# Performance work log

Measured on AMD Instinct MI355X. Metric: run time of the kernel, lower is better.

## Reference

```python
import jax, jax.numpy as jnp
import numpy as np

N_ATOMS = 30000
N_PAIRS = 1200000
N_BASIS = 7
N_RADIAL = 5
N_SPECIES = 119
R_MIN = 0.5
R_MAX = 6.0
UNITS = (512, 512)
BOX = 6.0  # Angstrom box edge so many pairs fall inside the cutoff
N_FEAT = 360  # gaussian-moment feature count for n_radial=5

# static triangular index sets (fully symmetric contractions)
_TRI2_I, _TRI2_J = np.triu_indices(N_RADIAL)
_TRI3 = np.array([(i, j, k) for i in range(N_RADIAL)
                  for j in range(i, N_RADIAL)
                  for k in range(j, N_RADIAL)], dtype=np.int32)


def setup_inputs() -> dict:
    key = jax.random.key(0)
    ks = jax.random.split(key, 8)
    R = jax.random.uniform(ks[0], (N_ATOMS, 3), jnp.float32) * BOX
    Z = jax.random.randint(ks[1], (N_ATOMS,), 0, N_SPECIES, dtype=jnp.int32)
    idx = jax.random.randint(ks[2], (2, N_PAIRS), 0, N_ATOMS, dtype=jnp.int32)
    W_radial = jax.random.normal(ks[3], (N_SPECIES, N_SPECIES, N_RADIAL, N_BASIS), jnp.float32) / np.sqrt(N_BASIS)
    w1 = jax.random.normal(ks[4], (N_FEAT, UNITS[0]), jnp.float32) / np.sqrt(N_FEAT)
    b1 = jnp.zeros((UNITS[0],), jnp.float32)
    w2 = jax.random.normal(ks[5], (UNITS[0], UNITS[1]), jnp.float32) / np.sqrt(UNITS[0])
    b2 = jnp.zeros((UNITS[1],), jnp.float32)
    w3 = jax.random.normal(ks[6], (UNITS[1], 1), jnp.float32) / np.sqrt(UNITS[1])
    b3 = jnp.zeros((1,), jnp.float32)
    scale = 2.0 * jnp.ones((N_SPECIES, 1), jnp.float32)
    shift = 1.0 * jnp.ones((N_SPECIES, 1), jnp.float32)
    return dict(R=R, Z=Z, idx=idx, W_radial=W_radial, w1=w1, b1=b1,
                w2=w2, b2=b2, w3=w3, b3=b3, scale=scale, shift=shift)


def _descriptor(R, Z, idx, W_radial):
    idx_i, idx_j = idx[0], idx[1]
    # pairwise displacement (free-space displacement fn)
    dr_vec = R[idx_j] - R[idx_i]                                  # [P,3]
    dr = jnp.sqrt(jnp.sum(dr_vec * dr_vec, axis=-1) + 1e-12)      # [P]
    dn = dr_vec / (dr + 1e-5)[:, None]                            # unit vectors [P,3]

    # gaussian radial basis
    betta = N_BASIS ** 2 / R_MAX ** 2
    rad_norm = (2.0 * betta / np.pi) ** 0.25
    shifts = R_MIN + (R_MAX - R_MIN) / N_BASIS * jnp.arange(N_BASIS, dtype=jnp.float32)
    basis = rad_norm * jnp.exp(-betta * (dr[:, None] - shifts) ** 2)  # [P,B]

    # cosine cutoff and per species-pair embedding of the basis
    cutoff = 0.5 * (jnp.cos(jnp.pi * dr / R_MAX) + 1.0) * (dr < R_MAX)
    coeffs = W_radial[Z[idx_i], Z[idx_j]]                          # [P,K,B] irregular gather
    radial = jnp.einsum('pkb,pb->pk', coeffs, basis)               # [P,K]
    radial = radial * (cutoff / np.sqrt(N_BASIS))[:, None]

    seg = lambda x: jax.ops.segment_sum(x, idx_i, num_segments=N_ATOMS)
    # geometric moments of order 0..3
    m0 = seg(radial)                                               # [A,K]
    m1 = seg(radial[:, :, None] * dn[:, None, :])                  # [A,K,3]
    dn2 = dn[:, :, None] * dn[:, None, :]                          # [P,3,3]
    m2 = seg(radial[:, :, None, None] * dn2[:, None])              # [A,K,3,3]
    dn3 = dn2[:, :, :, None] * dn[:, None, None, :]                # [P,3,3,3]
    m3 = seg(radial[:, :, None, None, None] * dn3[:, None])        # [A,K,3,3,3]

    # gaussian-moment invariant contractions
    c1 = jnp.einsum('ari,asi->ars', m1, m1)
    c2 = jnp.einsum('arij,asij->ars', m2, m2)
    c3 = jnp.einsum('arijk,asijk->ars', m3, m3)
    c4 = jnp.einsum('arij,asik,atjk->arst', m2, m2, m2)
    c5 = jnp.einsum('ari,asj,atij->arst', m1, m1, m2)
    c6 = jnp.einsum('arijk,asijl,atkl->arst', m3, m3, m2)
    c7 = jnp.einsum('arijk,asij,atk->arst', m3, m2, m1)

    A = m0.shape[0]
    gm = jnp.concatenate([
        m0,
        c1[:, _TRI2_I, _TRI2_J],
        c2[:, _TRI2_I, _TRI2_J],
        c3[:, _TRI2_I, _TRI2_J],
        c4[:, _TRI3[:, 0], _TRI3[:, 1], _TRI3[:, 2]],
        c5[:, _TRI2_I, _TRI2_J, :].reshape(A, -1),
        c6[:, _TRI2_I, _TRI2_J, :].reshape(A, -1),
        c7.reshape(A, -1),
    ], axis=-1)                                                    # [A,360]
    return gm


def reference(R, Z, idx, W_radial, w1, b1, w2, b2, w3, b3, scale, shift):
    gm = _descriptor(R, Z, idx, W_radial)
    h = jax.nn.swish(gm @ w1 + b1)
    h = jax.nn.swish(h @ w2 + b2)
    h = h @ w3 + b3                                                # [A,1]
    return scale[Z] * h + shift[Z]
```

## Files before the change

### kernel.cpp

```cpp
#include <hip/hip_runtime.h>

#define NA      30000
#define MPAD    30080
#define NPAIRS  1200000
#define NB      7
#define NK      5
#define NSP     119
#define NFEAT   360
#define KP1     384
#define NU      512
#define WROW    36
#define MAXSLOT 120
#define PSTRIDE 128
#define NBK     118
#define BCAP    11520
#define PPB     4688
#define NTILE   235

#define BETTA      1.3611111111111112f
#define RADNORM    0.96481348f
#define SHIFT_STEP 0.7857142857142857f
#define PI_OVER_R  0.5235987755982988f
#define INV_SQRT7  0.3779644730092272f
#define RMAXV      6.0f

typedef __attribute__((ext_vector_type(8))) short bf16x8;
typedef __attribute__((ext_vector_type(4))) float f32x4;

__device__ __forceinline__ unsigned short f2b(float x) {
    unsigned u = __float_as_uint(x);
    unsigned r = u + 0x7FFF + ((u >> 16) & 1);
    return (unsigned short)(r >> 16);
}

__global__ __launch_bounds__(256)
void k_part(const int* __restrict__ idx, const int* __restrict__ Z,
            int* __restrict__ gcur, int* __restrict__ part) {
    __shared__ int hist[NBK];
    __shared__ int base[NBK];
    int tid = threadIdx.x;
    for (int b = tid; b < NBK; b += 256) hist[b] = 0;
    __syncthreads();
    int p0 = blockIdx.x * PPB;
    int p1 = min(p0 + PPB, NPAIRS);
    for (int p = p0 + tid; p < p1; p += 256)
        atomicAdd(&hist[idx[p] >> 8], 1);
    __syncthreads();
    for (int b = tid; b < NBK; b += 256) {
        base[b] = atomicAdd(&gcur[b], hist[b]);
        hist[b] = 0;
    }
    __syncthreads();
    for (int p = p0 + tid; p < p1; p += 256) {
        int i = idx[p];
        int b = i >> 8;
        int j = idx[NPAIRS + p];
        int zj = Z[j];
        int off = base[b] + atomicAdd(&hist[b], 1);
        if (off < BCAP)
            part[b * BCAP + off] = ((i & 255) << 22) | (zj << 15) | j;
    }
}

__global__ __launch_bounds__(256)
void k_csr(const int* __restrict__ part, const int* __restrict__ gcnt,
           int* __restrict__ counts, int* __restrict__ plist) {
    __shared__ int lp[128 * MAXSLOT];
    __shared__ int lc[128];
    int tid = threadIdx.x;
    int lane = tid & 63, wave = tid >> 6;
    int w = blockIdx.x;
    int cb = w >> 1;
    int par = w & 1;
    for (int t = tid; t < 128; t += 256) lc[t] = 0;
    __syncthreads();
    int n = min(gcnt[cb], BCAP);
    for (int e = tid; e < n; e += 256) {
        int v = part[cb * BCAP + e];
        int iloc = v >> 22;
        if ((iloc >> 7) == par) {
            int i7 = iloc & 127;
            int r = atomicAdd(&lc[i7], 1);
            if (r < MAXSLOT) lp[i7 * MAXSLOT + r] = v & 0x3FFFFF;
        }
    }
    __syncthreads();
    for (int t = tid; t < 128; t += 256) {
        int a = w * 128 + t;
        if (a < NA) counts[a] = min(lc[t], MAXSLOT);
    }
    for (int rr = 0; rr < 32; rr++) {
        int row = wave * 32 + rr;
        int a = w * 128 + row;
        if (a < NA) {
            for (int c = lane; c < MAXSLOT; c += 64)
                plist[(size_t)a * PSTRIDE + c] = lp[row * MAXSLOT + c];
        }
    }
}

#define PREP_W   (NSP*NSP*WROW)
#define PREP_R   NA
#define PREP_W1  (NU*KP1)
#define PREP_W2  (NU*NU)
#define PREP_TOT (PREP_W + PREP_R + PREP_W1 + PREP_W2)
__global__ void k_prep(const float* __restrict__ W, const float* __restrict__ R,
                       const float* __restrict__ w1, const float* __restrict__ w2,
                       float* __restrict__ Wp, float* __restrict__ Rp,
                       unsigned short* __restrict__ w1T, unsigned short* __restrict__ w2T) {
    int i = blockIdx.x * blockDim.x + threadIdx.x;
    if (i < PREP_W) {
        int row = i / WROW, e = i - row * WROW;
        Wp[i] = (e < NK * NB) ? W[row * (NK * NB) + e] : 0.f;
        return;
    }
    i -= PREP_W;
    if (i < PREP_R) {
        f32x4 v = {R[3*i], R[3*i+1], R[3*i+2], 0.f};
        *(f32x4*)&Rp[4*i] = v;
        return;
    }
    i -= PREP_R;
    if (i < PREP_W1) {
        int c = i / KP1, kp = i - c * KP1;
        w1T[i] = (kp < NFEAT) ? f2b(w1[kp * NU + c]) : (unsigned short)0;
        return;
    }
    i -= PREP_W1;
    if (i < PREP_W2) {
        int c = i >> 9, kp = i & 511;
        w2T[i] = f2b(w2[kp * NU + c]);
    }
}

__global__ __launch_bounds__(256, 2)
void k_moments(const float* __restrict__ Rp, const int* __restrict__ Z,
               const float* __restrict__ Wp,
               const int* __restrict__ counts,
               const int* __restrict__ plist, float* __restrict__ MT) {
    int tid = blockIdx.x * blockDim.x + threadIdx.x;
    int a = tid >> 3, q = tid & 7;
    if (a >= NA) return;
    f32x4 ri = *(const f32x4*)&Rp[4*a];
    int Zi = Z[a];
    float acc[100];
#pragma unroll
    for (int u = 0; u < 100; u++) acc[u] = 0.f;
    int cnt = min(counts[a], MAXSLOT);
    const int* prow = plist + (size_t)a * PSTRIDE;
    for (int t = q; t < cnt; t += 8) {
        int pk = prow[t];
        int j  = pk & 0x7FFF;
        int Zj = (pk >> 15) & 0x7F;
        f32x4 rj = *(const f32x4*)&Rp[4*j];
        float dx = rj.x - ri.x, dy = rj.y - ri.y, dz = rj.z - ri.z;
        float d2 = dx*dx + dy*dy + dz*dz + 1e-12f;
        float dr = sqrtf(d2);
        float inv = 1.0f / (dr + 1e-5f);
        float nx = dx*inv, ny = dy*inv, nz = dz*inv;

        const f32x4* wrow = (const f32x4*)&Wp[(Zi * NSP + Zj) * WROW];
        f32x4 w4[9];
#pragma unroll
        for (int c = 0; c < 9; c++) w4[c] = wrow[c];
        const float* wf = (const float*)w4;

        float basis[NB];
#pragma unroll
        for (int b = 0; b < NB; b++) {
            float tt = dr - (0.5f + SHIFT_STEP * (float)b);
            basis[b] = RADNORM * __expf(-BETTA * tt * tt);
        }
        float cut = (dr < RMAXV) ? 0.5f * (__cosf(PI_OVER_R * dr) + 1.0f) : 0.0f;
        cut *= INV_SQRT7;
        float rad[NK];
#pragma unroll
        for (int k = 0; k < NK; k++) {
            float s = 0.f;
#pragma unroll
            for (int b = 0; b < NB; b++) s += wf[k*NB + b] * basis[b];
            rad[k] = s * cut;
        }
        float g[20];
        g[0] = 1.f; g[1] = nx; g[2] = ny; g[3] = nz;
        g[4] = nx*nx; g[5] = nx*ny; g[6] = nx*nz; g[7] = ny*ny; g[8] = ny*nz; g[9] = nz*nz;
        g[10] = g[4]*nx; g[11] = g[4]*ny; g[12] = g[4]*nz; g[13] = g[5]*ny; g[14] = g[5]*nz;
        g[15] = g[6]*nz; g[16] = g[7]*ny; g[17] = g[7]*nz; g[18] = g[8]*nz; g[19] = g[9]*nz;
#pragma unroll
        for (int k = 0; k < NK; k++)
#pragma unroll
            for (int u = 0; u < 20; u++)
                acc[k*20 + u] += rad[k] * g[u];
    }
#pragma unroll
    for (int u = 0; u < 100; u++) {
        float v = acc[u];
        v += __shfl_xor(v, 1);
        v += __shfl_xor(v, 2);
        v += __shfl_xor(v, 4);
        acc[u] = v;
    }
    if (q == 0) {
#pragma unroll
        for (int u = 0; u < 100; u++) MT[u * NA + a] = acc[u];
    }
}

__global__ __launch_bounds__(256)
void k_contract(const float* __restrict__ MT, unsigned short* __restrict__ gmB) {
    __shared__ float M[100 * 64];
    int tid = threadIdx.x;
    int lane = tid & 63;
    int wave = tid >> 6;
    int a0 = blockIdx.x * 64;
    int a = a0 + lane;

    for (int e = tid; e < 6400; e += 256) {
        int u = e >> 6, l = e & 63;
        int aa = a0 + l;
        M[e] = (aa < NA) ? MT[u * NA + aa] : 0.f;
    }
    __syncthreads();

    const int S2[3][3] = {{0,1,2},{1,3,4},{2,4,5}};
    const int S3[3][3][3] = {
        {{0,1,2},{1,3,4},{2,4,5}},
        {{1,3,4},{3,6,7},{4,7,8}},
        {{2,4,5},{4,7,8},{5,8,9}}
    };
    bool ok = (a < NA);
    unsigned short* row = gmB + (size_t)a * KP1;
#define LD(comp) M[(comp) * 64 + lane]

    if (wave == 0) {
        if (ok) {
            for (int k = 0; k < 5; k++) row[k] = f2b(LD(k * 20));
        }
        int f = 5;
        for (int r = 0; r < 5; r++)
            for (int s = r; s < 5; s++) {
                float v = 0.f;
#pragma unroll
                for (int i = 0; i < 3; i++) v += LD(r*20+1+i) * LD(s*20+1+i);
                if (ok) row[f] = f2b(v);
                f++;
            }
        const float W2U[6] = {1,2,2,1,2,1};
        for (int r = 0; r < 5; r++)
            for (int s = r; s < 5; s++) {
                float v = 0.f;
#pragma unroll
                for (int u = 0; u < 6; u++) v += W2U[u] * LD(r*20+4+u) * LD(s*20+4+u);
                if (ok) row[f] = f2b(v);
                f++;
            }
        const float W3U[10] = {1,3,3,3,6,3,1,3,3,1};
        for (int r = 0; r < 5; r++)
            for (int s = r; s < 5; s++) {
                float v = 0.f;
#pragma unroll
                for (int u = 0; u < 10; u++) v += W3U[u] * LD(r*20+10+u) * LD(s*20+10+u);
                if (ok) row[f] = f2b(v);
                f++;
            }
        for (int r = 0; r < 5; r++) {
            float m2r[6];
#pragma unroll
            for (int u = 0; u < 6; u++) m2r[u] = LD(r*20+4+u);
            for (int s = r; s < 5; s++) {
                float m2q[6];
#pragma unroll
                for (int u = 0; u < 6; u++) m2q[u] = LD(s*20+4+u);
                for (int t = s; t < 5; t++) {
                    float m2t[6];
#pragma unroll
                    for (int u = 0; u < 6; u++) m2t[u] = LD(t*20+4+u);
                    float v = 0.f;
#pragma unroll
                    for (int i = 0; i < 3; i++)
#pragma unroll
                        for (int j = 0; j < 3; j++)
#pragma unroll
                            for (int k = 0; k < 3; k++)
                                v += m2r[S2[i][j]] * m2q[S2[i][k]] * m2t[S2[j][k]];
                    if (ok) row[f] = f2b(v);
                    f++;
                }
            }
        }
    } else if (wave == 1) {
        int f = 85;
        for (int r = 0; r < 5; r++) {
            float m1r[3];
#pragma unroll
            for (int i = 0; i < 3; i++) m1r[i] = LD(r*20+1+i);
            for (int s = r; s < 5; s++) {
                float m1q[3];
#pragma unroll
                for (int i = 0; i < 3; i++) m1q[i] = LD(s*20+1+i);
                for (int t = 0; t < 5; t++) {
                    float m2t[6];
#pragma unroll
                    for (int u = 0; u < 6; u++) m2t[u] = LD(t*20+4+u);
                    float v = 0.f;
#pragma unroll
                    for (int i = 0; i < 3; i++)
#pragma unroll
                        for (int j = 0; j < 3; j++)
                            v += m1r[i] * m1q[j] * m2t[S2[i][j]];
                    if (ok) row[f] = f2b(v);
                    f++;
                }
            }
        }
        f = 235;
        for (int r = 0; r < 5; r++) {
            float m3r[10];
#pragma unroll
            for (int u = 0; u < 10; u++) m3r[u] = LD(r*20+10+u);
            for (int s = 0; s < 5; s++) {
                float m2q[6];
#pragma unroll
                for (int u = 0; u < 6; u++) m2q[u] = LD(s*20+4+u);
                float U0 = 0.f, U1 = 0.f, U2 = 0.f;
#pragma unroll
                for (int i = 0; i < 3; i++)
#pragma unroll
                    for (int j = 0; j < 3; j++) {
                        float ww = m2q[S2[i][j]];
                        U0 += m3r[S3[i][j][0]] * ww;
                        U1 += m3r[S3[i][j][1]] * ww;
                        U2 += m3r[S3[i][j][2]] * ww;
                    }
                for (int t = 0; t < 5; t++) {
                    float v = U0 * LD(t*20+1) + U1 * LD(t*20+2) + U2 * LD(t*20+3);
                    if (ok) row[f] = f2b(v);
                    f++;
                }
            }
        }
    } else {
        int pbeg = (wave == 2) ? 0 : 7;
        int pend = (wave == 2) ? 7 : 15;
        int p = 0;
        for (int r = 0; r < 5; r++)
            for (int s = r; s < 5; s++) {
                if (p >= pbeg && p < pend) {
                    float m3r[10], m3q[10];
#pragma unroll
                    for (int u = 0; u < 10; u++) m3r[u] = LD(r*20+10+u);
#pragma unroll
                    for (int u = 0; u < 10; u++) m3q[u] = LD(s*20+10+u);
                    float T[3][3];
#pragma unroll
                    for (int k = 0; k < 3; k++)
#pragma unroll
                        for (int l = 0; l < 3; l++) {
                            float v = 0.f;
#pragma unroll
                            for (int i = 0; i < 3; i++)
#pragma unroll
                                for (int j = 0; j < 3; j++)
                                    v += m3r[S3[i][j][k]] * m3q[S3[i][j][l]];
                            T[k][l] = v;
                        }
                    int f = 160 + p * 5;
                    for (int t = 0; t < 5; t++) {
                        float m2t[6];
#pragma unroll
                        for (int u = 0; u < 6; u++) m2t[u] = LD(t*20+4+u);
                        float v = 0.f;
#pragma unroll
                        for (int k = 0; k < 3; k++)
#pragma unroll
                            for (int l = 0; l < 3; l++)
                                v += T[k][l] * m2t[S2[k][l]];
                        if (ok) row[f + t] = f2b(v);
                    }
                }
                p++;
            }
        if (wave == 3 && ok) {
            for (int z = NFEAT; z < KP1; z++) row[z] = 0;
        }
    }
#undef LD
}

__device__ __forceinline__ void stage8(const unsigned short* gp, unsigned short* lp) {
    __builtin_amdgcn_global_load_lds(
        (const __attribute__((address_space(1))) unsigned int*)gp,
        (__attribute__((address_space(3))) unsigned int*)lp, 16, 0, 0);
}

template<int KPAD, int MODE>
__global__ __launch_bounds__(256) void k_mfma(const unsigned short* __restrict__ A,
                                              const unsigned short* __restrict__ B,
                                              const float* __restrict__ bias,
                                              const float* __restrict__ w3,
                                              void* __restrict__ outp) {
    __shared__ __align__(16) unsigned char SMEM[35072];
    unsigned short* As = (unsigned short*)SMEM;
    unsigned short* Bs = (unsigned short*)(SMEM + 16384);
    float* red = (float*)(SMEM + 32768);
    int tid = threadIdx.x;
    int lane = tid & 63, wave = tid >> 6;
    int wm = wave >> 1, wn = wave & 1;
    int quad = lane >> 4, l16 = lane & 15;
    int lrow = lane >> 3;
    int lchk = lane & 7;

    for (int t = 0; t < 2; t++) {
        int atile = blockIdx.y * 2 + t;
        if (atile >= NTILE) break;
        int rowA0, rowB0;
        if (MODE == 1) { rowA0 = atile * 128;      rowB0 = blockIdx.x * 128; }
        else           { rowA0 = blockIdx.x * 128; rowB0 = atile * 128; }

        f32x4 acc[4][4];
        f32x4 zero = {0.f, 0.f, 0.f, 0.f};
#pragma unroll
        for (int i = 0; i < 4; i++)
#pragma unroll
            for (int j = 0; j < 4; j++) acc[i][j] = zero;

        for (int k0 = 0; k0 < KPAD; k0 += 64) {
            __syncthreads();
#pragma unroll
            for (int i = 0; i < 4; i++) {
                int r = wave * 32 + i * 8 + lrow;
                int gc = lchk ^ (r & 7);
                stage8(A + (size_t)(rowA0 + r) * KPAD + k0 + gc * 8, &As[(wave * 32 + i * 8) * 64]);
            }
#pragma unroll
            for (int i = 0; i < 4; i++) {
                int r = wave * 32 + i * 8 + lrow;
                int gc = lchk ^ (r & 7);
                stage8(B + (size_t)(rowB0 + r) * KPAD + k0 + gc * 8, &Bs[(wave * 32 + i * 8) * 64]);
            }
            __syncthreads();
#pragma unroll
            for (int s = 0; s < 2; s++) {
                bf16x8 af[4], bfr[4];
#pragma unroll
                for (int mt = 0; mt < 4; mt++) {
                    int r = wm * 64 + mt * 16 + l16;
                    af[mt] = *(const bf16x8*)&As[r * 64 + (((s * 4 + quad) ^ (r & 7)) * 8)];
                }
#pragma unroll
                for (int nt = 0; nt < 4; nt++) {
                    int r = wn * 64 + nt * 16 + l16;
                    bfr[nt] = *(const bf16x8*)&Bs[r * 64 + (((s * 4 + quad) ^ (r & 7)) * 8)];
                }
#pragma unroll
                for (int mt = 0; mt < 4; mt++)
#pragma unroll
                    for (int nt = 0; nt < 4; nt++)
                        acc[mt][nt] = __builtin_amdgcn_mfma_f32_16x16x32_bf16(
                            af[mt], bfr[nt], acc[mt][nt], 0, 0, 0);
            }
        }

        if (MODE == 1) {
            __syncthreads();
            unsigned short* Ot = (unsigned short*)SMEM;
#pragma unroll
            for (int nt = 0; nt < 4; nt++) {
                int c_loc = wn * 64 + nt * 16 + l16;
                float b = bias[rowB0 + c_loc];
#pragma unroll
                for (int mt = 0; mt < 4; mt++) {
#pragma unroll
                    for (int reg = 0; reg < 4; reg++) {
                        int a_loc = wm * 64 + mt * 16 + quad * 4 + reg;
                        float v = acc[mt][nt][reg] + b;
                        Ot[a_loc * 136 + c_loc] = f2b(v / (1.f + __expf(-v)));
                    }
                }
            }
            __syncthreads();
            unsigned short* O = (unsigned short*)outp;
            int half = lane >> 5, l32 = lane & 31;
#pragma unroll
            for (int it = 0; it < 16; it++) {
                int rloc = wave * 32 + it * 2 + half;
                int a = rowA0 + rloc;
                unsigned long long d = *(const unsigned long long*)&Ot[rloc * 136 + l32 * 4];
                if (a < NA)
                    *(unsigned long long*)&O[(size_t)a * NU + rowB0 + l32 * 4] = d;
            }
        } else {
            float pn[4] = {0.f, 0.f, 0.f, 0.f};
#pragma unroll
            for (int mt = 0; mt < 4; mt++) {
#pragma unroll
                for (int reg = 0; reg < 4; reg++) {
                    int c = rowA0 + wm * 64 + mt * 16 + quad * 4 + reg;
                    float b = bias[c];
                    float w3c = w3[c];
#pragma unroll
                    for (int nt = 0; nt < 4; nt++) {
                        float v = acc[mt][nt][reg] + b;
                        pn[nt] += w3c * (v / (1.f + __expf(-v)));
                    }
                }
            }
#pragma unroll
            for (int nt = 0; nt < 4; nt++) {
                pn[nt] += __shfl_xor(pn[nt], 16);
                pn[nt] += __shfl_xor(pn[nt], 32);
            }
            __syncthreads();
            if (quad == 0) {
#pragma unroll
                for (int nt = 0; nt < 4; nt++)
                    red[((wm * 2 + wn) * 4 + nt) * 16 + l16] = pn[nt];
            }
            __syncthreads();
            if (tid < 128) {
                int wn2 = tid >> 6, nt2 = (tid >> 4) & 3, lb = tid & 15;
                float s = red[((0 * 2 + wn2) * 4 + nt2) * 16 + lb]
                        + red[((1 * 2 + wn2) * 4 + nt2) * 16 + lb];
                int a = rowB0 + wn2 * 64 + nt2 * 16 + lb;
                if (a < NA) atomicAdd((float*)outp + a, s);
            }
        }
    }
}

__global__ void k_finish(float* __restrict__ out, const float* __restrict__ b3,
                         const int* __restrict__ Z, const float* __restrict__ scale,
                         const float* __restrict__ shift) {
    int a = blockIdx.x * blockDim.x + threadIdx.x;
    if (a >= NA) return;
    int z = Z[a];
    out[a] = scale[z] * (out[a] + b3[0]) + shift[z];
}

extern "C" void kernel_launch(void* const* d_in, const int* in_sizes, int n_in,
                              void* d_out, int out_size, void* d_ws, size_t ws_size,
                              hipStream_t stream) {
    const float* R    = (const float*)d_in[0];
    const int*   Z    = (const int*)  d_in[1];
    const int*   idx  = (const int*)  d_in[2];
    const float* Wr   = (const float*)d_in[3];
    const float* w1   = (const float*)d_in[4];
    const float* b1   = (const float*)d_in[5];
    const float* w2   = (const float*)d_in[6];
    const float* b2   = (const float*)d_in[7];
    const float* w3   = (const float*)d_in[8];
    const float* b3   = (const float*)d_in[9];
    const float* scale= (const float*)d_in[10];
    const float* shift= (const float*)d_in[11];
    float* out = (float*)d_out;
    char* ws = (char*)d_ws;

    int*            gcur   = (int*)  (ws + 0);
    int*            counts = (int*)  (ws + 512);
    int*            part   = (int*)  (ws + 120576);
    int*            plist  = (int*)  (ws + 5558016);
    float*          MT     = (float*)(ws + 20918016);
    unsigned short* gmB    = (unsigned short*)(ws + 32918016);
    unsigned short* w1T    = (unsigned short*)(ws + 56019456);
    unsigned short* w2T    = (unsigned short*)(ws + 56412672);
    unsigned short* h1B    = (unsigned short*)(ws + 56936960);
    float*          Wpad   = (float*)(ws + 87738880);
    float*          Rpad   = (float*)(ws + 89778064);

    hipMemsetAsync(gcur, 0, 512, stream);
    hipMemsetAsync(d_out, 0, NA * sizeof(float), stream);

    k_part    <<<256, 256, 0, stream>>>(idx, Z, gcur, part);
    k_csr     <<<235, 256, 0, stream>>>(part, gcur, counts, plist);
    k_prep    <<<(PREP_TOT + 255) / 256, 256, 0, stream>>>(Wr, R, w1, w2, Wpad, Rpad, w1T, w2T);
    k_moments <<<(NA * 8 + 255) / 256, 256, 0, stream>>>(Rpad, Z, Wpad, counts, plist, MT);
    k_contract<<<(NA + 63) / 64,       256, 0, stream>>>(MT, gmB);

    k_mfma<KP1, 1><<<dim3(NU / 128, 118), 256, 0, stream>>>(gmB, w1T, b1, nullptr, (void*)h1B);
    k_mfma<NU,  2><<<dim3(NU / 128, 118), 256, 0, stream>>>(w2T, h1B, b2, w3, (void*)out);

    k_finish<<<(NA + 255) / 256, 256, 0, stream>>>(out, b3, Z, scale, shift);
}
```

Measured before the change: 271.0 us.

## Split per-atom moment accumulation across two 8-lane groups with partial buffers

Each atom in k_moments is now handled by 16 threads in two groups of 8. Each group writes its own partial moment buffer (MT0/MT1), and k_contract adds the two when it loads. The launch bound rises to 4 blocks per CU, the next pair index is prefetched, the W-row load moves ahead of the geometry math, and the final stores are spread across lanes. The intent is more parallelism and better latency hiding in the gather-heavy moment pass. The costs are lower register budget per thread for the 100-float accumulator, which risks spills, plus an extra partial buffer to write and read.

```diff
diff --git a/kernel.cpp b/kernel.cpp
--- a/kernel.cpp
+++ b/kernel.cpp
@@ -133,13 +133,14 @@
     }
 }
 
-__global__ __launch_bounds__(256, 2)
+__global__ __launch_bounds__(256, 4)
 void k_moments(const float* __restrict__ Rp, const int* __restrict__ Z,
                const float* __restrict__ Wp,
                const int* __restrict__ counts,
-               const int* __restrict__ plist, float* __restrict__ MT) {
+               const int* __restrict__ plist,
+               float* __restrict__ MT0, float* __restrict__ MT1) {
     int tid = blockIdx.x * blockDim.x + threadIdx.x;
-    int a = tid >> 3, q = tid & 7;
+    int a = tid >> 4, sub = (tid >> 3) & 1, q = tid & 7;
     if (a >= NA) return;
     f32x4 ri = *(const f32x4*)&Rp[4*a];
     int Zi = Z[a];
@@ -148,23 +149,28 @@
     for (int u = 0; u < 100; u++) acc[u] = 0.f;
     int cnt = min(counts[a], MAXSLOT);
     const int* prow = plist + (size_t)a * PSTRIDE;
-    for (int t = q; t < cnt; t += 8) {
-        int pk = prow[t];
+
+    int t = q + 8 * sub;
+    int pk = (t < cnt) ? prow[t] : 0;
+    while (t < cnt) {
+        int tn = t + 16;
+        int pk_next = (tn < cnt) ? prow[tn] : 0;
         int j  = pk & 0x7FFF;
         int Zj = (pk >> 15) & 0x7F;
         f32x4 rj = *(const f32x4*)&Rp[4*j];
+
+        const f32x4* wrow = (const f32x4*)&Wp[(Zi * NSP + Zj) * WROW];
+        f32x4 w4[9];
+#pragma unroll
+        for (int c = 0; c < 9; c++) w4[c] = wrow[c];
+        const float* wf = (const float*)w4;
+
         float dx = rj.x - ri.x, dy = rj.y - ri.y, dz = rj.z - ri.z;
         float d2 = dx*dx + dy*dy + dz*dz + 1e-12f;
         float dr = sqrtf(d2);
         float inv = 1.0f / (dr + 1e-5f);
         float nx = dx*inv, ny = dy*inv, nz = dz*inv;
 
-        const f32x4* wrow = (const f32x4*)&Wp[(Zi * NSP + Zj) * WROW];
-        f32x4 w4[9];
-#pragma unroll
-        for (int c = 0; c < 9; c++) w4[c] = wrow[c];
-        const float* wf = (const float*)w4;
-
         float basis[NB];
 #pragma unroll
         for (int b = 0; b < NB; b++) {
@@ -191,6 +197,8 @@
 #pragma unroll
             for (int u = 0; u < 20; u++)
                 acc[k*20 + u] += rad[k] * g[u];
+        t = tn;
+        pk = pk_next;
     }
 #pragma unroll
     for (int u = 0; u < 100; u++) {
@@ -200,14 +208,14 @@
         v += __shfl_xor(v, 4);
         acc[u] = v;
     }
-    if (q == 0) {
-#pragma unroll
-        for (int u = 0; u < 100; u++) MT[u * NA + a] = acc[u];
-    }
+    float* MT = sub ? MT1 : MT0;
+#pragma unroll
+    for (int u = q; u < 100; u += 8) MT[u * NA + a] = acc[u];
 }
 
 __global__ __launch_bounds__(256)
-void k_contract(const float* __restrict__ MT, unsigned short* __restrict__ gmB) {
+void k_contract(const float* __restrict__ MT0, const float* __restrict__ MT1,
+                unsigned short* __restrict__ gmB) {
     __shared__ float M[100 * 64];
     int tid = threadIdx.x;
     int lane = tid & 63;
@@ -218,7 +226,7 @@
     for (int e = tid; e < 6400; e += 256) {
         int u = e >> 6, l = e & 63;
         int aa = a0 + l;
-        M[e] = (aa < NA) ? MT[u * NA + aa] : 0.f;
+        M[e] = (aa < NA) ? MT0[u * NA + aa] + MT1[u * NA + aa] : 0.f;
     }
     __syncthreads();
 
@@ -559,13 +567,14 @@
     int*            counts = (int*)  (ws + 512);
     int*            part   = (int*)  (ws + 120576);
     int*            plist  = (int*)  (ws + 5558016);
-    float*          MT     = (float*)(ws + 20918016);
+    float*          MT0    = (float*)(ws + 20918016);
     unsigned short* gmB    = (unsigned short*)(ws + 32918016);
     unsigned short* w1T    = (unsigned short*)(ws + 56019456);
     unsigned short* w2T    = (unsigned short*)(ws + 56412672);
     unsigned short* h1B    = (unsigned short*)(ws + 56936960);
     float*          Wpad   = (float*)(ws + 87738880);
     float*          Rpad   = (float*)(ws + 89778064);
+    float*          MT1    = (float*)(ws + 90258064);
 
     hipMemsetAsync(gcur, 0, 512, stream);
     hipMemsetAsync(d_out, 0, NA * sizeof(float), stream);
@@ -573,8 +582,8 @@
     k_part    <<<256, 256, 0, stream>>>(idx, Z, gcur, part);
     k_csr     <<<235, 256, 0, stream>>>(part, gcur, counts, plist);
     k_prep    <<<(PREP_TOT + 255) / 256, 256, 0, stream>>>(Wr, R, w1, w2, Wpad, Rpad, w1T, w2T);
-    k_moments <<<(NA * 8 + 255) / 256, 256, 0, stream>>>(Rpad, Z, Wpad, counts, plist, MT);
-    k_contract<<<(NA + 63) / 64,       256, 0, stream>>>(MT, gmB);
+    k_moments <<<(NA * 16 + 255) / 256, 256, 0, stream>>>(Rpad, Z, Wpad, counts, plist, MT0, MT1);
+    k_contract<<<(NA + 63) / 64,       256, 0, stream>>>(MT0, MT1, gmB);
 
     k_mfma<KP1, 1><<<dim3(NU / 128, 118), 256, 0, stream>>>(gmB, w1T, b1, nullptr, (void*)h1B);
     k_mfma<NU,  2><<<dim3(NU / 128, 118), 256, 0, stream>>>(w2T, h1B, b2, w3, (void*)out);
```

Result: slower. 442.8 us (+63.4%).

## Split per-pair radial/direction computation into separate fully-parallel kernel with fp16 staging

Applied to the files above, without the earlier changes.

Moves the per-pair work (distance, Gaussian basis, cutoff, species-weighted radial contraction, unit vector) out of the moment accumulation kernel into a new one-thread-per-pair kernel. That kernel writes 5 radial values and 3 direction components as fp16 into a staging buffer, which the moments kernel then reads and accumulates. The aim is to relieve the register-heavy accumulation kernel (2 waves per SIMD) of the scattered loads and transcendental math, so that work runs at higher occupancy. The cost is an extra launch, about 61 MB of staging writes and reads, and lower precision from fp16. The MAXSLOT clamp on counts was also removed from the moments kernel.

```diff
diff --git a/kernel.cpp b/kernel.cpp
--- a/kernel.cpp
+++ b/kernel.cpp
@@ -26,6 +26,7 @@
 
 typedef __attribute__((ext_vector_type(8))) short bf16x8;
 typedef __attribute__((ext_vector_type(4))) float f32x4;
+typedef __attribute__((ext_vector_type(8))) _Float16 f16x8;
 
 __device__ __forceinline__ unsigned short f2b(float x) {
     unsigned u = __float_as_uint(x);
@@ -133,54 +134,71 @@
     }
 }
 
+__global__ __launch_bounds__(256)
+void k_pair(const float* __restrict__ Rp, const int* __restrict__ Z,
+            const float* __restrict__ Wp, const int* __restrict__ counts,
+            const int* __restrict__ plist, f16x8* __restrict__ pairH) {
+    int id = blockIdx.x * 256 + threadIdx.x;
+    if (id >= NA * PSTRIDE) return;
+    int a = id >> 7, s = id & 127;
+    if (s >= counts[a]) return;
+    int pk = plist[id];
+    int j  = pk & 0x7FFF;
+    int Zj = (pk >> 15) & 0x7F;
+    f32x4 ri = *(const f32x4*)&Rp[4*a];
+    f32x4 rj = *(const f32x4*)&Rp[4*j];
+    int Zi = Z[a];
+
+    const f32x4* wrow = (const f32x4*)&Wp[(Zi * NSP + Zj) * WROW];
+    f32x4 w4[9];
+#pragma unroll
+    for (int c = 0; c < 9; c++) w4[c] = wrow[c];
+    const float* wf = (const float*)w4;
+
+    float dx = rj.x - ri.x, dy = rj.y - ri.y, dz = rj.z - ri.z;
+    float d2 = dx*dx + dy*dy + dz*dz + 1e-12f;
+    float dr = sqrtf(d2);
+    float inv = 1.0f / (dr + 1e-5f);
+    float nx = dx*inv, ny = dy*inv, nz = dz*inv;
+
+    float basis[NB];
+#pragma unroll
+    for (int b = 0; b < NB; b++) {
+        float tt = dr - (0.5f + SHIFT_STEP * (float)b);
+        basis[b] = RADNORM * __expf(-BETTA * tt * tt);
+    }
+    float cut = (dr < RMAXV) ? 0.5f * (__cosf(PI_OVER_R * dr) + 1.0f) : 0.0f;
+    cut *= INV_SQRT7;
+    f16x8 o;
+#pragma unroll
+    for (int k = 0; k < NK; k++) {
+        float ssum = 0.f;
+#pragma unroll
+        for (int b = 0; b < NB; b++) ssum += wf[k*NB + b] * basis[b];
+        o[k] = (_Float16)(ssum * cut);
+    }
+    o[5] = (_Float16)nx; o[6] = (_Float16)ny; o[7] = (_Float16)nz;
+    pairH[id] = o;
+}
+
 __global__ __launch_bounds__(256, 2)
-void k_moments(const float* __restrict__ Rp, const int* __restrict__ Z,
-               const float* __restrict__ Wp,
-               const int* __restrict__ counts,
-               const int* __restrict__ plist, float* __restrict__ MT) {
+void k_moments(const int* __restrict__ counts, const f16x8* __restrict__ pairH,
+               float* __restrict__ MT) {
     int tid = blockIdx.x * blockDim.x + threadIdx.x;
     int a = tid >> 3, q = tid & 7;
     if (a >= NA) return;
-    f32x4 ri = *(const f32x4*)&Rp[4*a];
-    int Zi = Z[a];
     float acc[100];
 #pragma unroll
     for (int u = 0; u < 100; u++) acc[u] = 0.f;
-    int cnt = min(counts[a], MAXSLOT);
-    const int* prow = plist + (size_t)a * PSTRIDE;
+    int cnt = counts[a];
+    const f16x8* prow = pairH + a * PSTRIDE;
+
     for (int t = q; t < cnt; t += 8) {
-        int pk = prow[t];
-        int j  = pk & 0x7FFF;
-        int Zj = (pk >> 15) & 0x7F;
-        f32x4 rj = *(const f32x4*)&Rp[4*j];
-        float dx = rj.x - ri.x, dy = rj.y - ri.y, dz = rj.z - ri.z;
-        float d2 = dx*dx + dy*dy + dz*dz + 1e-12f;
-        float dr = sqrtf(d2);
-        float inv = 1.0f / (dr + 1e-5f);
-        float nx = dx*inv, ny = dy*inv, nz = dz*inv;
-
-        const f32x4* wrow = (const f32x4*)&Wp[(Zi * NSP + Zj) * WROW];
-        f32x4 w4[9];
-#pragma unroll
-        for (int c = 0; c < 9; c++) w4[c] = wrow[c];
-        const float* wf = (const float*)w4;
-
-        float basis[NB];
-#pragma unroll
-        for (int b = 0; b < NB; b++) {
-            float tt = dr - (0.5f + SHIFT_STEP * (float)b);
-            basis[b] = RADNORM * __expf(-BETTA * tt * tt);
-        }
-        float cut = (dr < RMAXV) ? 0.5f * (__cosf(PI_OVER_R * dr) + 1.0f) : 0.0f;
-        cut *= INV_SQRT7;
+        f16x8 pv = prow[t];
         float rad[NK];
 #pragma unroll
-        for (int k = 0; k < NK; k++) {
-            float s = 0.f;
-#pragma unroll
-            for (int b = 0; b < NB; b++) s += wf[k*NB + b] * basis[b];
-            rad[k] = s * cut;
-        }
+        for (int k = 0; k < NK; k++) rad[k] = (float)pv[k];
+        float nx = (float)pv[5], ny = (float)pv[6], nz = (float)pv[7];
         float g[20];
         g[0] = 1.f; g[1] = nx; g[2] = ny; g[3] = nz;
         g[4] = nx*nx; g[5] = nx*ny; g[6] = nx*nz; g[7] = ny*ny; g[8] = ny*nz; g[9] = nz*nz;
@@ -566,6 +584,7 @@
     unsigned short* h1B    = (unsigned short*)(ws + 56936960);
     float*          Wpad   = (float*)(ws + 87738880);
     float*          Rpad   = (float*)(ws + 89778064);
+    f16x8*          pairH  = (f16x8*)(ws + 90258064);
 
     hipMemsetAsync(gcur, 0, 512, stream);
     hipMemsetAsync(d_out, 0, NA * sizeof(float), stream);
@@ -573,7 +592,8 @@
     k_part    <<<256, 256, 0, stream>>>(idx, Z, gcur, part);
     k_csr     <<<235, 256, 0, stream>>>(part, gcur, counts, plist);
     k_prep    <<<(PREP_TOT + 255) / 256, 256, 0, stream>>>(Wr, R, w1, w2, Wpad, Rpad, w1T, w2T);
-    k_moments <<<(NA * 8 + 255) / 256, 256, 0, stream>>>(Rpad, Z, Wpad, counts, plist, MT);
+    k_pair    <<<(NA * PSTRIDE) / 256, 256, 0, stream>>>(Rpad, Z, Wpad, counts, plist, pairH);
+    k_moments <<<(NA * 8 + 255) / 256, 256, 0, stream>>>(counts, pairH, MT);
     k_contract<<<(NA + 63) / 64,       256, 0, stream>>>(MT, gmB);
 
     k_mfma<KP1, 1><<<dim3(NU / 128, 118), 256, 0, stream>>>(gmB, w1T, b1, nullptr, (void*)h1B);
```

After: 278.4 us. 1.03x slower.

## Split moment kernel into pair-staging phase and LDS-fed accumulation phase

Applied to the files above, without the earlier changes.

k_moments now runs in two phases per block of 32 atoms. First, threads gather neighbour positions and weights, compute the radial terms and unit vectors, and store them as fp16 in a swizzled 64 KB shared-memory buffer. Then they read those back to build the 100 moment accumulators. The aim is to keep the latency-bound gathers apart from the register-heavy accumulation loop, so more loads can be in flight. The costs are the large LDS footprint, a block barrier, fp16 rounding of the radial values and directions, and dropping the MAXSLOT clamp in the read phase.

```diff
diff --git a/kernel.cpp b/kernel.cpp
--- a/kernel.cpp
+++ b/kernel.cpp
@@ -26,6 +26,7 @@
 
 typedef __attribute__((ext_vector_type(8))) short bf16x8;
 typedef __attribute__((ext_vector_type(4))) float f32x4;
+typedef __attribute__((ext_vector_type(8))) _Float16 f16x8;
 
 __device__ __forceinline__ unsigned short f2b(float x) {
     unsigned u = __float_as_uint(x);
@@ -135,62 +136,92 @@
 
 __global__ __launch_bounds__(256, 2)
 void k_moments(const float* __restrict__ Rp, const int* __restrict__ Z,
-               const float* __restrict__ Wp,
-               const int* __restrict__ counts,
+               const float* __restrict__ Wp, const int* __restrict__ counts,
                const int* __restrict__ plist, float* __restrict__ MT) {
-    int tid = blockIdx.x * blockDim.x + threadIdx.x;
-    int a = tid >> 3, q = tid & 7;
+    __shared__ __align__(16) _Float16 PH[32 * 128 * 8];
+    int tid = threadIdx.x;
+    int a0 = blockIdx.x * 32;
+
+    {
+        int i  = tid >> 3;
+        int ls = tid & 7;
+        int a = a0 + i;
+        if (a < NA) {
+            int cnt = counts[a];
+            f32x4 ri = *(const f32x4*)&Rp[4*a];
+            int Zi = Z[a];
+            const int* prow = plist + (size_t)a * PSTRIDE;
+            int swz = i & 7;
+#pragma unroll 4
+            for (int k = 0; k < 16; k++) {
+                int s = ls + 8 * k;
+                if (s >= cnt) break;
+                int pk = prow[s];
+                int j  = pk & 0x7FFF;
+                int Zj = (pk >> 15) & 0x7F;
+                f32x4 rj = *(const f32x4*)&Rp[4*j];
+
+                const f32x4* wrow = (const f32x4*)&Wp[(Zi * NSP + Zj) * WROW];
+                f32x4 w4[9];
+#pragma unroll
+                for (int c = 0; c < 9; c++) w4[c] = wrow[c];
+                const float* wf = (const float*)w4;
+
+                float dx = rj.x - ri.x, dy = rj.y - ri.y, dz = rj.z - ri.z;
+                float d2 = dx*dx + dy*dy + dz*dz + 1e-12f;
+                float dr = sqrtf(d2);
+                float inv = 1.0f / (dr + 1e-5f);
+                float nx = dx*inv, ny = dy*inv, nz = dz*inv;
+
+                float basis[NB];
+#pragma unroll
+                for (int b = 0; b < NB; b++) {
+                    float tt = dr - (0.5f + SHIFT_STEP * (float)b);
+                    basis[b] = RADNORM * __expf(-BETTA * tt * tt);
+                }
+                float cut = (dr < RMAXV) ? 0.5f * (__cosf(PI_OVER_R * dr) + 1.0f) : 0.0f;
+                cut *= INV_SQRT7;
+                f16x8 o;
+#pragma unroll
+                for (int kk = 0; kk < NK; kk++) {
+                    float ssum = 0.f;
+#pragma unroll
+                    for (int b = 0; b < NB; b++) ssum += wf[kk*NB + b] * basis[b];
+                    o[kk] = (_Float16)(ssum * cut);
+                }
+                o[5] = (_Float16)nx; o[6] = (_Float16)ny; o[7] = (_Float16)nz;
+                int s_sw = (s & ~7) | ((s & 7) ^ swz);
+                *(f16x8*)&PH[(i * 128 + s_sw) * 8] = o;
+            }
+        }
+    }
+    __syncthreads();
+
+    int g = tid >> 3, q = tid & 7;
+    int a = a0 + g;
     if (a >= NA) return;
-    f32x4 ri = *(const f32x4*)&Rp[4*a];
-    int Zi = Z[a];
     float acc[100];
 #pragma unroll
     for (int u = 0; u < 100; u++) acc[u] = 0.f;
-    int cnt = min(counts[a], MAXSLOT);
-    const int* prow = plist + (size_t)a * PSTRIDE;
+    int cnt = counts[a];
+    int swz = g & 7;
     for (int t = q; t < cnt; t += 8) {
-        int pk = prow[t];
-        int j  = pk & 0x7FFF;
-        int Zj = (pk >> 15) & 0x7F;
-        f32x4 rj = *(const f32x4*)&Rp[4*j];
-        float dx = rj.x - ri.x, dy = rj.y - ri.y, dz = rj.z - ri.z;
-        float d2 = dx*dx + dy*dy + dz*dz + 1e-12f;
-        float dr = sqrtf(d2);
-        float inv = 1.0f / (dr + 1e-5f);
-        float nx = dx*inv, ny = dy*inv, nz = dz*inv;
-
-        const f32x4* wrow = (const f32x4*)&Wp[(Zi * NSP + Zj) * WROW];
-        f32x4 w4[9];
-#pragma unroll
-        for (int c = 0; c < 9; c++) w4[c] = wrow[c];
-        const float* wf = (const float*)w4;
-
-        float basis[NB];
-#pragma unroll
-        for (int b = 0; b < NB; b++) {
-            float tt = dr - (0.5f + SHIFT_STEP * (float)b);
-            basis[b] = RADNORM * __expf(-BETTA * tt * tt);
-        }
-        float cut = (dr < RMAXV) ? 0.5f * (__cosf(PI_OVER_R * dr) + 1.0f) : 0.0f;
-        cut *= INV_SQRT7;
+        int s_sw = (t & ~7) | ((t & 7) ^ swz);
+        f16x8 pv = *(const f16x8*)&PH[(g * 128 + s_sw) * 8];
         float rad[NK];
 #pragma unroll
-        for (int k = 0; k < NK; k++) {
-            float s = 0.f;
-#pragma unroll
-            for (int b = 0; b < NB; b++) s += wf[k*NB + b] * basis[b];
-            rad[k] = s * cut;
-        }
-        float g[20];
-        g[0] = 1.f; g[1] = nx; g[2] = ny; g[3] = nz;
-        g[4] = nx*nx; g[5] = nx*ny; g[6] = nx*nz; g[7] = ny*ny; g[8] = ny*nz; g[9] = nz*nz;
-        g[10] = g[4]*nx; g[11] = g[4]*ny; g[12] = g[4]*nz; g[13] = g[5]*ny; g[14] = g[5]*nz;
-        g[15] = g[6]*nz; g[16] = g[7]*ny; g[17] = g[7]*nz; g[18] = g[8]*nz; g[19] = g[9]*nz;
+        for (int k = 0; k < NK; k++) rad[k] = (float)pv[k];
+        float nx = (float)pv[5], ny = (float)pv[6], nz = (float)pv[7];
+        float gg[20];
+        gg[0] = 1.f; gg[1] = nx; gg[2] = ny; gg[3] = nz;
+        gg[4] = nx*nx; gg[5] = nx*ny; gg[6] = nx*nz; gg[7] = ny*ny; gg[8] = ny*nz; gg[9] = nz*nz;
+        gg[10] = gg[4]*nx; gg[11] = gg[4]*ny; gg[12] = gg[4]*nz; gg[13] = gg[5]*ny; gg[14] = gg[5]*nz;
+        gg[15] = gg[6]*nz; gg[16] = gg[7]*ny; gg[17] = gg[7]*nz; gg[18] = gg[8]*nz; gg[19] = gg[9]*nz;
 #pragma unroll
         for (int k = 0; k < NK; k++)
 #pragma unroll
             for (int u = 0; u < 20; u++)
-                acc[k*20 + u] += rad[k] * g[u];
+                acc[k*20 + u] += rad[k] * gg[u];
     }
 #pragma unroll
     for (int u = 0; u < 100; u++) {
@@ -573,7 +604,7 @@
     k_part    <<<256, 256, 0, stream>>>(idx, Z, gcur, part);
     k_csr     <<<235, 256, 0, stream>>>(part, gcur, counts, plist);
     k_prep    <<<(PREP_TOT + 255) / 256, 256, 0, stream>>>(Wr, R, w1, w2, Wpad, Rpad, w1T, w2T);
-    k_moments <<<(NA * 8 + 255) / 256, 256, 0, stream>>>(Rpad, Z, Wpad, counts, plist, MT);
+    k_moments <<<(NA + 31) / 32, 256, 0, stream>>>(Rpad, Z, Wpad, counts, plist, MT);
     k_contract<<<(NA + 63) / 64,       256, 0, stream>>>(MT, gmB);
 
     k_mfma<KP1, 1><<<dim3(NU / 128, 118), 256, 0, stream>>>(gmB, w1T, b1, nullptr, (void*)h1B);
```

Result: no change. 272.5 us (+0.6%).
